# Performance work log

Hardware: AMD Instinct MI355X
Metric: run time of the kernel (lower is better)

The kernel has to match this reference:

```python
import jax, jax.numpy as jnp
import numpy as np

B, C, T, F = 256, 1, 8192, 16


def _lrelu(h):
    return jnp.where(h > 0, h, 0.01 * h)


def _adain(h, style):
    # h: (B, T, 8), style: (B, 8, 2)
    scale = style[:, None, :, 0]          # (B, 1, 8)
    bias = style[:, None, :, 1]           # (B, 1, 8)
    mu = jnp.mean(h, axis=-1, keepdims=True)
    sigma = jnp.std(h, axis=-1, ddof=1, keepdims=True) + 1e-6  # torch.std is unbiased
    return scale * (h - mu) / sigma + bias


def setup_inputs() -> dict:
    key = jax.random.key(0)
    ks = jax.random.split(key, 20)
    g = lambda k, shp, s=0.2: (jax.random.normal(k, shp, dtype=jnp.float32) * s)
    inp = {
        "x": jax.random.normal(ks[0], (B, C, T), dtype=jnp.float32),
        "metadata": jax.random.normal(ks[1], (B, F), dtype=jnp.float32),
        # MetadataMLP: F->64->128->64 (total_channels*2 = 32*2)
        "mw1": g(ks[2], (F, 64)), "mb1": g(ks[3], (64,)),
        "mw2": g(ks[4], (64, 128)), "mb2": g(ks[5], (128,)),
        "mw3": g(ks[6], (128, 64)), "mb3": g(ks[7], (64,)),
        # main chain 1->8->8->8->8->1
        "w1": g(ks[8], (1, 8)), "b1": g(ks[9], (8,)),
        "w2": g(ks[10], (8, 8)), "b2": g(ks[11], (8,)),
        "w3": g(ks[12], (8, 8)), "b3": g(ks[13], (8,)),
        "w4": g(ks[14], (8, 8)), "b4": g(ks[15], (8,)),
        "w5": g(ks[16], (8, 1)), "b5": g(ks[17], (1,)),
    }
    return inp


def reference(x, metadata, mw1, mb1, mw2, mb2, mw3, mb3,
              w1, b1, w2, b2, w3, b3, w4, b4, w5, b5):
    # style MLP
    s = jax.nn.relu(metadata @ mw1 + mb1)
    s = jax.nn.relu(s @ mw2 + mb2)
    s = s @ mw3 + mb3                     # (B, 64)
    s1, s2, s3, s4 = jnp.split(s, 4, axis=1)  # each (B, 16)
    s1, s2, s3, s4 = (t.reshape(-1, 8, 2) for t in (s1, s2, s3, s4))

    h = jnp.transpose(x, (0, 2, 1))       # (B, T, 1)
    h = h @ w1 + b1                       # (B, T, 8)
    h = _lrelu(_adain(h, s1))
    h = h @ w2 + b2
    h = _lrelu(_adain(h, s2))
    h = h @ w3 + b3
    h = _lrelu(_adain(h, s3))
    h = h @ w4 + b4
    h = _lrelu(_adain(h, s4))
    h = h @ w5 + b5                       # (B, T, 1)
    out = _lrelu(h)
    return jnp.transpose(out, (0, 2, 1))  # (B, 1, T)
```

## Files before the change

kernel.cpp:

```cpp
#include <hip/hip_runtime.h>

#define BATCH  256
#define TLEN   8192
#define TPB    1024
#define LUTN   1024
#define VLO    -8.0f
#define H      0.015625f
#define INVH   64.0f
#define UOFF   512.0f
#define UMAX   1022.999f
#define SQRT7  2.6457513110645906f
#define C1     2.6457513110645906e-6f


__device__ __forceinline__ float rowmean8(const float* __restrict__ p) {
    return (((p[0] + p[1]) + (p[2] + p[3])) + ((p[4] + p[5]) + (p[6] + p[7]))) * 0.125f;
}
__device__ __forceinline__ float lrelu(float t) { return fmaxf(t, 0.01f * t); }

__device__ __forceinline__ void adain_layer(
    float h[8], const float* __restrict__ wl, const float* __restrict__ bl,
    const float* scp)
{
    float a[8];
    #pragma unroll
    for (int j = 0; j < 8; ++j) a[j] = bl[j];
    #pragma unroll
    for (int k = 0; k < 8; ++k) {
        const float hk = h[k];
        #pragma unroll
        for (int j = 0; j < 8; ++j) a[j] = fmaf(hk, wl[k * 8 + j], a[j]);
    }
    const float mu = (((a[0] + a[1]) + (a[2] + a[3])) +
                      ((a[4] + a[5]) + (a[6] + a[7]))) * 0.125f;
    float g[8], var = 0.f;
    #pragma unroll
    for (int j = 0; j < 8; ++j) { g[j] = a[j] - mu; var = fmaf(g[j], g[j], var); }
    const float r = __builtin_amdgcn_rcpf(__builtin_amdgcn_sqrtf(var) + C1);
    const float4 s0 = *(const float4*)(scp);
    const float4 s1 = *(const float4*)(scp + 4);
    const float4 t0 = *(const float4*)(scp + 8);
    const float4 t1 = *(const float4*)(scp + 12);
    const float sc[8] = {s0.x,s0.y,s0.z,s0.w,s1.x,s1.y,s1.z,s1.w};
    const float sb[8] = {t0.x,t0.y,t0.z,t0.w,t1.x,t1.y,t1.z,t1.w};
    #pragma unroll
    for (int j = 0; j < 8; ++j)
        h[j] = lrelu(fmaf(g[j] * r, sc[j], sb[j]));
}

__global__ __launch_bounds__(TPB, 8) void adain_lut_kernel(
    const float* __restrict__ x, const float* __restrict__ metadata,
    const float* __restrict__ mw1, const float* __restrict__ mb1,
    const float* __restrict__ mw2, const float* __restrict__ mb2,
    const float* __restrict__ mw3, const float* __restrict__ mb3,
    const float* __restrict__ w1, const float* __restrict__ b1,
    const float* __restrict__ w2, const float* __restrict__ b2,
    const float* __restrict__ w3, const float* __restrict__ b3,
    const float* __restrict__ w4, const float* __restrict__ b4,
    const float* __restrict__ w5, const float* __restrict__ b5,
    float* __restrict__ out)
{
    __shared__ float smw1[1024];
    __shared__ float smw2[8192];
    __shared__ float smw3[8192];
    __shared__ float md[16];
    __shared__ float h1[64];
    __shared__ float h2[128];
    __shared__ float s[64];
    __shared__ float la[8], lc[8];
    __shared__ float p[80];
    __shared__ float lut[LUTN];

    const int b   = blockIdx.x;
    const int tid = threadIdx.x;

    const int base4 = b * (TLEN / 4) + tid;
    float4 vx0 = ((const float4*)x)[base4];
    float4 vx1 = ((const float4*)x)[base4 + TPB];

    float4 t2a = ((const float4*)mw2)[tid];
    float4 t2b = ((const float4*)mw2)[tid + TPB];
    float4 t3a = ((const float4*)mw3)[tid];
    float4 t3b = ((const float4*)mw3)[tid + TPB];
    float4 t1  = (tid < 256) ? ((const float4*)mw1)[tid] : make_float4(0.f, 0.f, 0.f, 0.f);

    ((float4*)smw2)[tid]       = t2a;
    ((float4*)smw2)[tid + TPB] = t2b;
    ((float4*)smw3)[tid]       = t3a;
    ((float4*)smw3)[tid + TPB] = t3b;
    if (tid < 256) ((float4*)smw1)[tid] = t1;

    if (tid < 16) {
        md[tid] = metadata[b * 16 + tid];
    } else if (tid >= 64 && tid < 72) {
        int j = tid - 64; la[j] = w1[j] - rowmean8(w1); lc[j] = b1[j] - rowmean8(b1);
    } else if (tid == 80) {
        p[27] = b5[0];
    }
    __syncthreads();

    if (tid < 64) {
        float a = mb1[tid];
        #pragma unroll
        for (int k = 0; k < 16; ++k) a = fmaf(md[k], smw1[k * 64 + tid], a);
        h1[tid] = fmaxf(a, 0.f);
    }
    __syncthreads();
    if (tid < 128) {
        float a = mb2[tid];
        #pragma unroll 16
        for (int k = 0; k < 64; ++k) a = fmaf(h1[k], smw2[k * 128 + tid], a);
        h2[tid] = fmaxf(a, 0.f);
    }
    __syncthreads();
    if (tid < 64) {
        float a = mb3[tid];
        #pragma unroll 16
        for (int k = 0; k < 128; ++k) a = fmaf(h2[k], smw3[k * 64 + tid], a);
        s[tid] = a;
    }
    __syncthreads();

    if (tid < 8) {
        const float sc1 = s[2 * tid] * SQRT7;
        p[tid]      = la[tid] * sc1;
        p[8 + tid]  = lc[tid] * sc1;
        p[16 + tid] = s[2 * tid + 1];
        #pragma unroll
        for (int l = 0; l < 3; ++l) {
            p[28 + 16 * l + tid] = s[16 * (l + 1) + 2 * tid] * SQRT7;
            p[36 + 16 * l + tid] = s[16 * (l + 1) + 2 * tid + 1];
        }
    } else if (tid == 8) {
        float A = 0.f, Bv = 0.f, Cv = 0.f;
        #pragma unroll
        for (int j = 0; j < 8; ++j) {
            A  = fmaf(la[j], la[j], A);
            Bv = fmaf(la[j], lc[j], Bv);
            Cv = fmaf(lc[j], lc[j], Cv);
        }
        p[24] = A; p[25] = 2.f * Bv; p[26] = Cv;
    }
    __syncthreads();

    {
        const float4 q = *(const float4*)(p + 24);
        const float vv = VLO + (float)tid * H;

        float h[8];
        {
            const float4 a0 = *(const float4*)(p);
            const float4 a1 = *(const float4*)(p + 4);
            const float4 c0 = *(const float4*)(p + 8);
            const float4 c1 = *(const float4*)(p + 12);
            const float4 s0 = *(const float4*)(p + 16);
            const float4 s1 = *(const float4*)(p + 20);
            const float laa[8] = {a0.x,a0.y,a0.z,a0.w,a1.x,a1.y,a1.z,a1.w};
            const float lcc[8] = {c0.x,c0.y,c0.z,c0.w,c1.x,c1.y,c1.z,c1.w};
            const float sb1[8] = {s0.x,s0.y,s0.z,s0.w,s1.x,s1.y,s1.z,s1.w};
            const float var = fmaxf(fmaf(vv, fmaf(vv, q.x, q.y), q.z), 0.f);
            const float r   = __builtin_amdgcn_rcpf(__builtin_amdgcn_sqrtf(var) + C1);
            #pragma unroll
            for (int j = 0; j < 8; ++j) {
                const float d = fmaf(vv, laa[j], lcc[j]);
                h[j] = lrelu(fmaf(d, r, sb1[j]));
            }
        }

        adain_layer(h, w2, b2, p + 28);
        adain_layer(h, w3, b3, p + 44);
        adain_layer(h, w4, b4, p + 60);

        {
            float a = q.w;
            #pragma unroll
            for (int k = 0; k < 8; ++k) a = fmaf(h[k], w5[k], a);
            lut[tid] = lrelu(a);
        }
    }
    __syncthreads();

    #pragma unroll
    for (int r = 0; r < 2; ++r) {
        const float4 v = r ? vx1 : vx0;
        const float vin[4] = {v.x, v.y, v.z, v.w};
        float vo[4];
        #pragma unroll
        for (int c = 0; c < 4; ++c) {
            float u = fmaf(vin[c], INVH, UOFF);
            u = fminf(fmaxf(u, 0.0f), UMAX);
            const int   i = (int)u;
            const float f = u - (float)i;
            const float a = lut[i];
            const float d = lut[i + 1] - a;
            vo[c] = fmaf(f, d, a);
        }
        ((float4*)out)[base4 + r * TPB] = make_float4(vo[0], vo[1], vo[2], vo[3]);
    }
}

extern "C" void kernel_launch(void* const* d_in, const int* in_sizes, int n_in,
                              void* d_out, int out_size, void* d_ws, size_t ws_size,
                              hipStream_t stream)
{
    const float* x        = (const float*)d_in[0];
    const float* metadata = (const float*)d_in[1];
    const float* mw1      = (const float*)d_in[2];
    const float* mb1      = (const float*)d_in[3];
    const float* mw2      = (const float*)d_in[4];
    const float* mb2      = (const float*)d_in[5];
    const float* mw3      = (const float*)d_in[6];
    const float* mb3      = (const float*)d_in[7];
    const float* w1       = (const float*)d_in[8];
    const float* b1       = (const float*)d_in[9];
    const float* w2       = (const float*)d_in[10];
    const float* b2       = (const float*)d_in[11];
    const float* w3       = (const float*)d_in[12];
    const float* b3       = (const float*)d_in[13];
    const float* w4       = (const float*)d_in[14];
    const float* b4       = (const float*)d_in[15];
    const float* w5       = (const float*)d_in[16];
    const float* b5       = (const float*)d_in[17];

    adain_lut_kernel<<<BATCH, TPB, 0, stream>>>(
        x, metadata, mw1, mb1, mw2, mb2, mw3, mb3,
        w1, b1, w2, b2, w3, b3, w4, b4, w5, b5, (float*)d_out);
}
```

Baseline: 101.4 us.

## Compute style MLP from register-held weights with shuffle reductions, drop shared staging

```diff
diff --git a/kernel.cpp b/kernel.cpp
--- a/kernel.cpp
+++ b/kernel.cpp
@@ -13,14 +13,11 @@
 #define C1     2.6457513110645906e-6f
 
 
-__device__ __forceinline__ float rowmean8(const float* __restrict__ p) {
-    return (((p[0] + p[1]) + (p[2] + p[3])) + ((p[4] + p[5]) + (p[6] + p[7]))) * 0.125f;
-}
 __device__ __forceinline__ float lrelu(float t) { return fmaxf(t, 0.01f * t); }
 
 __device__ __forceinline__ void adain_layer(
     float h[8], const float* __restrict__ wl, const float* __restrict__ bl,
-    const float* scp)
+    const float* ssl)
 {
     float a[8];
     #pragma unroll
@@ -37,18 +34,12 @@
     #pragma unroll
     for (int j = 0; j < 8; ++j) { g[j] = a[j] - mu; var = fmaf(g[j], g[j], var); }
     const float r = __builtin_amdgcn_rcpf(__builtin_amdgcn_sqrtf(var) + C1);
-    const float4 s0 = *(const float4*)(scp);
-    const float4 s1 = *(const float4*)(scp + 4);
-    const float4 t0 = *(const float4*)(scp + 8);
-    const float4 t1 = *(const float4*)(scp + 12);
-    const float sc[8] = {s0.x,s0.y,s0.z,s0.w,s1.x,s1.y,s1.z,s1.w};
-    const float sb[8] = {t0.x,t0.y,t0.z,t0.w,t1.x,t1.y,t1.z,t1.w};
     #pragma unroll
     for (int j = 0; j < 8; ++j)
-        h[j] = lrelu(fmaf(g[j] * r, sc[j], sb[j]));
+        h[j] = lrelu(fmaf(g[j] * r, ssl[2 * j] * SQRT7, ssl[2 * j + 1]));
 }
 
-__global__ __launch_bounds__(TPB, 8) void adain_lut_kernel(
+__global__ __launch_bounds__(TPB, 4) void adain_lut_kernel(
     const float* __restrict__ x, const float* __restrict__ metadata,
     const float* __restrict__ mw1, const float* __restrict__ mb1,
     const float* __restrict__ mw2, const float* __restrict__ mb2,
@@ -60,123 +51,107 @@
     const float* __restrict__ w5, const float* __restrict__ b5,
     float* __restrict__ out)
 {
-    __shared__ float smw1[1024];
-    __shared__ float smw2[8192];
-    __shared__ float smw3[8192];
-    __shared__ float md[16];
-    __shared__ float h1[64];
-    __shared__ float h2[128];
-    __shared__ float s[64];
-    __shared__ float la[8], lc[8];
-    __shared__ float p[80];
+    __shared__ float h1s[64];
+    __shared__ float h2s[128];
+    __shared__ float ss[64];
     __shared__ float lut[LUTN];
 
-    const int b   = blockIdx.x;
-    const int tid = threadIdx.x;
+    const int b    = blockIdx.x;
+    const int tid  = threadIdx.x;
+    const int lane = tid & 63;
 
     const int base4 = b * (TLEN / 4) + tid;
-    float4 vx0 = ((const float4*)x)[base4];
-    float4 vx1 = ((const float4*)x)[base4 + TPB];
-
-    float4 t2a = ((const float4*)mw2)[tid];
-    float4 t2b = ((const float4*)mw2)[tid + TPB];
-    float4 t3a = ((const float4*)mw3)[tid];
-    float4 t3b = ((const float4*)mw3)[tid + TPB];
-    float4 t1  = (tid < 256) ? ((const float4*)mw1)[tid] : make_float4(0.f, 0.f, 0.f, 0.f);
-
-    ((float4*)smw2)[tid]       = t2a;
-    ((float4*)smw2)[tid + TPB] = t2b;
-    ((float4*)smw3)[tid]       = t3a;
-    ((float4*)smw3)[tid + TPB] = t3b;
-    if (tid < 256) ((float4*)smw1)[tid] = t1;
-
-    if (tid < 16) {
-        md[tid] = metadata[b * 16 + tid];
-    } else if (tid >= 64 && tid < 72) {
-        int j = tid - 64; la[j] = w1[j] - rowmean8(w1); lc[j] = b1[j] - rowmean8(b1);
-    } else if (tid == 80) {
-        p[27] = b5[0];
-    }
-    __syncthreads();
+    const float4 vx0 = ((const float4*)x)[base4];
+    const float4 vx1 = ((const float4*)x)[base4 + TPB];
+
+    const int j2 = tid >> 3, kk2 = tid & 7;
+    float wr2[8];
+    #pragma unroll
+    for (int i = 0; i < 8; ++i) wr2[i] = mw2[(kk2 + 8 * i) * 128 + j2];
+    const float bias2 = mb2[j2];
+
+    const int j3 = tid >> 4, kk3 = tid & 15;
+    float wr3[8];
+    #pragma unroll
+    for (int i = 0; i < 8; ++i) wr3[i] = mw3[(kk3 + 16 * i) * 64 + j3];
+    const float bias3 = mb3[j3];
 
     if (tid < 64) {
-        float a = mb1[tid];
-        #pragma unroll
-        for (int k = 0; k < 16; ++k) a = fmaf(md[k], smw1[k * 64 + tid], a);
-        h1[tid] = fmaxf(a, 0.f);
-    }
-    __syncthreads();
-    if (tid < 128) {
-        float a = mb2[tid];
-        #pragma unroll 16
-        for (int k = 0; k < 64; ++k) a = fmaf(h1[k], smw2[k * 128 + tid], a);
-        h2[tid] = fmaxf(a, 0.f);
-    }
-    __syncthreads();
-    if (tid < 64) {
-        float a = mb3[tid];
-        #pragma unroll 16
-        for (int k = 0; k < 128; ++k) a = fmaf(h2[k], smw3[k * 64 + tid], a);
-        s[tid] = a;
-    }
-    __syncthreads();
-
-    if (tid < 8) {
-        const float sc1 = s[2 * tid] * SQRT7;
-        p[tid]      = la[tid] * sc1;
-        p[8 + tid]  = lc[tid] * sc1;
-        p[16 + tid] = s[2 * tid + 1];
-        #pragma unroll
-        for (int l = 0; l < 3; ++l) {
-            p[28 + 16 * l + tid] = s[16 * (l + 1) + 2 * tid] * SQRT7;
-            p[36 + 16 * l + tid] = s[16 * (l + 1) + 2 * tid + 1];
-        }
-    } else if (tid == 8) {
+        const float mdv = (lane < 16) ? metadata[b * 16 + lane] : 0.f;
+        float w1col[16];
+        #pragma unroll
+        for (int k = 0; k < 16; ++k) w1col[k] = mw1[k * 64 + lane];
+        float a = mb1[lane];
+        #pragma unroll
+        for (int k = 0; k < 16; ++k) a = fmaf(__shfl(mdv, k), w1col[k], a);
+        h1s[lane] = fmaxf(a, 0.f);
+    }
+    __syncthreads();
+
+    {
+        float acc = 0.f;
+        #pragma unroll
+        for (int i = 0; i < 8; ++i) acc = fmaf(h1s[kk2 + 8 * i], wr2[i], acc);
+        acc += __shfl_xor(acc, 1);
+        acc += __shfl_xor(acc, 2);
+        acc += __shfl_xor(acc, 4);
+        if (kk2 == 0) h2s[j2] = fmaxf(acc + bias2, 0.f);
+    }
+    __syncthreads();
+
+    {
+        float acc = 0.f;
+        #pragma unroll
+        for (int i = 0; i < 8; ++i) acc = fmaf(h2s[kk3 + 16 * i], wr3[i], acc);
+        acc += __shfl_xor(acc, 1);
+        acc += __shfl_xor(acc, 2);
+        acc += __shfl_xor(acc, 4);
+        acc += __shfl_xor(acc, 8);
+        if (kk3 == 0) ss[j3] = acc + bias3;
+    }
+    __syncthreads();
+
+    {
+        float w1v[8], b1v[8];
+        #pragma unroll
+        for (int j = 0; j < 8; ++j) { w1v[j] = w1[j]; b1v[j] = b1[j]; }
+        const float mw = (((w1v[0] + w1v[1]) + (w1v[2] + w1v[3])) +
+                          ((w1v[4] + w1v[5]) + (w1v[6] + w1v[7]))) * 0.125f;
+        const float mb = (((b1v[0] + b1v[1]) + (b1v[2] + b1v[3])) +
+                          ((b1v[4] + b1v[5]) + (b1v[6] + b1v[7]))) * 0.125f;
+        float la[8], lc[8];
         float A = 0.f, Bv = 0.f, Cv = 0.f;
         #pragma unroll
         for (int j = 0; j < 8; ++j) {
+            la[j] = w1v[j] - mw;
+            lc[j] = b1v[j] - mb;
             A  = fmaf(la[j], la[j], A);
             Bv = fmaf(la[j], lc[j], Bv);
             Cv = fmaf(lc[j], lc[j], Cv);
         }
-        p[24] = A; p[25] = 2.f * Bv; p[26] = Cv;
-    }
-    __syncthreads();
-
-    {
-        const float4 q = *(const float4*)(p + 24);
-        const float vv = VLO + (float)tid * H;
+        const float B2  = 2.f * Bv;
+        const float b5v = b5[0];
+
+        const float vv  = VLO + (float)tid * H;
+        const float var = fmaxf(fmaf(vv, fmaf(vv, A, B2), Cv), 0.f);
+        const float r   = __builtin_amdgcn_rcpf(__builtin_amdgcn_sqrtf(var) + C1);
 
         float h[8];
-        {
-            const float4 a0 = *(const float4*)(p);
-            const float4 a1 = *(const float4*)(p + 4);
-            const float4 c0 = *(const float4*)(p + 8);
-            const float4 c1 = *(const float4*)(p + 12);
-            const float4 s0 = *(const float4*)(p + 16);
-            const float4 s1 = *(const float4*)(p + 20);
-            const float laa[8] = {a0.x,a0.y,a0.z,a0.w,a1.x,a1.y,a1.z,a1.w};
-            const float lcc[8] = {c0.x,c0.y,c0.z,c0.w,c1.x,c1.y,c1.z,c1.w};
-            const float sb1[8] = {s0.x,s0.y,s0.z,s0.w,s1.x,s1.y,s1.z,s1.w};
-            const float var = fmaxf(fmaf(vv, fmaf(vv, q.x, q.y), q.z), 0.f);
-            const float r   = __builtin_amdgcn_rcpf(__builtin_amdgcn_sqrtf(var) + C1);
-            #pragma unroll
-            for (int j = 0; j < 8; ++j) {
-                const float d = fmaf(vv, laa[j], lcc[j]);
-                h[j] = lrelu(fmaf(d, r, sb1[j]));
-            }
+        #pragma unroll
+        for (int j = 0; j < 8; ++j) {
+            const float sc1 = ss[2 * j] * SQRT7;
+            const float d   = fmaf(vv, la[j], lc[j]) * sc1;
+            h[j] = lrelu(fmaf(d, r, ss[2 * j + 1]));
         }
 
-        adain_layer(h, w2, b2, p + 28);
-        adain_layer(h, w3, b3, p + 44);
-        adain_layer(h, w4, b4, p + 60);
-
-        {
-            float a = q.w;
-            #pragma unroll
-            for (int k = 0; k < 8; ++k) a = fmaf(h[k], w5[k], a);
-            lut[tid] = lrelu(a);
-        }
+        adain_layer(h, w2, b2, ss + 16);
+        adain_layer(h, w3, b3, ss + 32);
+        adain_layer(h, w4, b4, ss + 48);
+
+        float a = b5v;
+        #pragma unroll
+        for (int k = 0; k < 8; ++k) a = fmaf(h[k], w5[k], a);
+        lut[tid] = lrelu(a);
     }
     __syncthreads();
 
```

Measured after the change: 104.5 us. 3.0% more time.
